# Kernel tuning notes

Measured on AMD Instinct MI355X. Metric: run time of the kernel, lower is better.

Reference implementation:

```python
import jax, jax.numpy as jnp
import numpy as np

N = 4096
IN_DIM, HID, OUT_DIM = 512, 256, 64
PROP_STEP = 10
LAM_HAT = 0.9
SCAD_A = 3.7
EPS = 1e-8


def setup_inputs() -> dict:
    key = jax.random.key(0)
    kA, kF, k1, k2 = jax.random.split(key, 4)
    # sparse symmetric 0/1 adjacency, zero diagonal (add_loops adds I later)
    u = jax.random.uniform(kA, (N, N), dtype=jnp.float32)
    A = (u < 0.005).astype(jnp.float32)
    A = jnp.maximum(A, A.T)
    A = A * (1.0 - jnp.eye(N, dtype=jnp.float32))
    F = jax.random.normal(kF, (N, IN_DIM), dtype=jnp.float32)
    W1 = jax.random.normal(k1, (IN_DIM, HID), dtype=jnp.float32) / np.sqrt(IN_DIM)
    b1 = jnp.zeros((HID,), dtype=jnp.float32)
    W2 = jax.random.normal(k2, (HID, OUT_DIM), dtype=jnp.float32) / np.sqrt(HID)
    b2 = jnp.zeros((OUT_DIM,), dtype=jnp.float32)
    raw_gamma = jnp.zeros((PROP_STEP,), dtype=jnp.float32)
    return {"A": A, "F": F, "W1": W1, "b1": b1, "W2": W2, "b2": b2,
            "raw_gamma": raw_gamma}


def reference(A, F, W1, b1, W2, b2, raw_gamma):
    lam = 1.0 / LAM_HAT - 1.0
    a = SCAD_A
    # MLP (dropout inactive at inference)
    F0 = jax.nn.relu(F @ W1 + b1) @ W2 + b2            # [N, out_dim]
    eye = jnp.eye(A.shape[0], dtype=A.dtype)
    A = A + eye                                        # add_loops
    D = A.sum(-1)                                      # [N]
    D_sq = jnp.sqrt(D)[:, None]                        # [N, 1]
    A_tilde = A / D_sq / D_sq.T                        # sym_norm: D^-1/2 A D^-1/2
    gammas = jax.nn.sigmoid(raw_gamma) * 2.0           # per-layer gamma in (0, 2)

    def step(Fc, gamma_k):
        Fn = Fc / D_sq
        nrm = jnp.linalg.norm(Fn, axis=-1, keepdims=True)
        Fu = Fn / jnp.maximum(nrm, 1e-12)
        # cosine distance in [0, 2]; detached as in torch (.detach())
        y = jax.lax.stop_gradient(1.0 - Fu @ Fu.T)     # [N, N]
        lam_k = jnp.maximum(gamma_k / a, EPS)
        t = a * lam_k
        safe_y = jnp.where(y <= 0.0, 1.0, y)
        w_mid = (t - y) / ((a - 1.0) * safe_y)
        # SCAD weight: 1 for y<=lam_k, linear decay on [lam_k, a*lam_k], 0 beyond
        W = jnp.where(y <= lam_k, 1.0, jnp.where(y <= t, w_mid, 0.0))
        W = W * (1.0 - eye)
        W = jnp.where(jnp.isnan(W), 1.0, W)
        Q_hat = ((W * A).sum(-1) / D + lam)[:, None]   # [N, 1]
        F_new = (W * A_tilde) @ Fc / Q_hat + lam * F0 / Q_hat
        return F_new, None

    F_out, _ = jax.lax.scan(step, F0, gammas)
    return F_out
```

## Files before the change

### kernel.cpp

```cpp
#include <hip/hip_runtime.h>
#include <hip/hip_bf16.h>

#define N_NODES 4096
#define IN_DIM  512
#define HID_DIM 256
#define OUT_DIM 64
#define PROP_STEP 10
#define MAX_DEG 128
#define KSPLIT  4
#define LAM_CONST (1.0f/0.9f - 1.0f)
#define SCAD_A 3.7f

__device__ __forceinline__ ushort f2bf(float f) {
    unsigned u = __float_as_uint(f);
    unsigned r = (u + 0x7FFFu + ((u >> 16) & 1u)) >> 16;
    return (ushort)r;
}
__device__ __forceinline__ unsigned pack2(float lo, float hi) {
    return (unsigned)f2bf(lo) | ((unsigned)f2bf(hi) << 16);
}
__device__ __forceinline__ float bflo(unsigned u) { return __uint_as_float(u << 16); }
__device__ __forceinline__ float bfhi(unsigned u) { return __uint_as_float(u & 0xFFFF0000u); }

__device__ __forceinline__ float wave_reduce_add(float v) {
#pragma unroll
    for (int off = 32; off > 0; off >>= 1) v += __shfl_xor(v, off, 64);
    return v;
}

__global__ __launch_bounds__(256) void build_graph(
    const float* __restrict__ A, int* __restrict__ ell, int* __restrict__ deg,
    float* __restrict__ invD, float* __restrict__ invDsq)
{
    int i = blockIdx.x;
    int t = threadIdx.x;
    __shared__ int cnt;
    if (t == 0) cnt = 0;
    __syncthreads();
    const float4* row = (const float4*)(A + (size_t)i * N_NODES);
    for (int q = t; q < N_NODES / 4; q += 256) {
        float4 v = row[q];
        if (v.x != 0.0f) { int p = atomicAdd(&cnt, 1); if (p < MAX_DEG) ell[i * MAX_DEG + p] = q * 4 + 0; }
        if (v.y != 0.0f) { int p = atomicAdd(&cnt, 1); if (p < MAX_DEG) ell[i * MAX_DEG + p] = q * 4 + 1; }
        if (v.z != 0.0f) { int p = atomicAdd(&cnt, 1); if (p < MAX_DEG) ell[i * MAX_DEG + p] = q * 4 + 2; }
        if (v.w != 0.0f) { int p = atomicAdd(&cnt, 1); if (p < MAX_DEG) ell[i * MAX_DEG + p] = q * 4 + 3; }
    }
    __syncthreads();
    if (t == 0) {
        int c = cnt;
        if (c > MAX_DEG) c = MAX_DEG;
        deg[i] = c;
        int pad = (c + 15) & ~15;
        if (pad > MAX_DEG) pad = MAX_DEG;
        for (int p = c; p < pad; p++) ell[i * MAX_DEG + p] = i;
        float d = (float)(cnt + 1);
        invD[i] = 1.0f / d;
        invDsq[i] = rsqrtf(d);
    }
}

__global__ __launch_bounds__(256) void mlp1(
    const float* __restrict__ F, const float* __restrict__ W1,
    float* __restrict__ Hp)
{
    __shared__ float sA[16][68];
    __shared__ float sB[16][68];
    int t  = threadIdx.x;
    int m0 = blockIdx.x * 64;
    int n0 = blockIdx.y * 64;
    int kp = blockIdx.z;
    int tm = (t & 15) * 4;
    int tn = (t >> 4) * 4;
    int ar = t >> 2;
    int ac = (t & 3) * 4;
    int br = t >> 4;
    int bc = (t & 15) * 4;
    float acc[4][4] = {};
    int k0 = kp * (IN_DIM / KSPLIT);
    for (int kc = k0; kc < k0 + IN_DIM / KSPLIT; kc += 16) {
        float4 va = *(const float4*)(F  + (size_t)(m0 + ar) * IN_DIM + kc + ac);
        float4 vb = *(const float4*)(W1 + (size_t)(kc + br) * HID_DIM + n0 + bc);
        __syncthreads();
        sA[ac + 0][ar] = va.x;
        sA[ac + 1][ar] = va.y;
        sA[ac + 2][ar] = va.z;
        sA[ac + 3][ar] = va.w;
        *(float4*)&sB[br][bc] = vb;
        __syncthreads();
#pragma unroll
        for (int k = 0; k < 16; k++) {
            float4 a = *(const float4*)&sA[k][tm];
            float4 b = *(const float4*)&sB[k][tn];
            acc[0][0] += a.x * b.x; acc[0][1] += a.x * b.y; acc[0][2] += a.x * b.z; acc[0][3] += a.x * b.w;
            acc[1][0] += a.y * b.x; acc[1][1] += a.y * b.y; acc[1][2] += a.y * b.z; acc[1][3] += a.y * b.w;
            acc[2][0] += a.z * b.x; acc[2][1] += a.z * b.y; acc[2][2] += a.z * b.z; acc[2][3] += a.z * b.w;
            acc[3][0] += a.w * b.x; acc[3][1] += a.w * b.y; acc[3][2] += a.w * b.z; acc[3][3] += a.w * b.w;
        }
    }
    float* Hb = Hp + (size_t)kp * N_NODES * HID_DIM;
#pragma unroll
    for (int r = 0; r < 4; r++) {
        *(float4*)&Hb[(size_t)(m0 + tm + r) * HID_DIM + n0 + tn] =
            make_float4(acc[r][0], acc[r][1], acc[r][2], acc[r][3]);
    }
}

__global__ __launch_bounds__(256) void reduce_H(
    float* __restrict__ Hp, const float* __restrict__ b1)
{
    size_t idx = (size_t)blockIdx.x * 256 + threadIdx.x;
    const size_t PS = (size_t)N_NODES * HID_DIM / 4;
    float4* H4 = (float4*)Hp;
    float4 s0 = H4[idx], s1 = H4[idx + PS], s2 = H4[idx + 2 * PS], s3 = H4[idx + 3 * PS];
    int col4 = (int)((idx * 4) & (HID_DIM - 1));
    float4 bb = *(const float4*)(b1 + col4);
    float4 o;
    o.x = fmaxf(s0.x + s1.x + s2.x + s3.x + bb.x, 0.0f);
    o.y = fmaxf(s0.y + s1.y + s2.y + s3.y + bb.y, 0.0f);
    o.z = fmaxf(s0.z + s1.z + s2.z + s3.z + bb.z, 0.0f);
    o.w = fmaxf(s0.w + s1.w + s2.w + s3.w + bb.w, 0.0f);
    H4[idx] = o;
}

__global__ __launch_bounds__(256) void mlp2(
    const float* __restrict__ H, const float* __restrict__ W2,
    const float* __restrict__ b2, const float* __restrict__ invDsq,
    float* __restrict__ F0, unsigned* __restrict__ P0)
{
    int wid = threadIdx.x >> 6, lane = threadIdx.x & 63;
    int row = blockIdx.x * 4 + wid;
    const float* h = H + (size_t)row * HID_DIM;
    float acc = b2[lane];
    for (int k = 0; k < HID_DIM; k += 4) {
        float4 hv = *(const float4*)(h + k);
        acc += hv.x * W2[(k + 0) * OUT_DIM + lane];
        acc += hv.y * W2[(k + 1) * OUT_DIM + lane];
        acc += hv.z * W2[(k + 2) * OUT_DIM + lane];
        acc += hv.w * W2[(k + 3) * OUT_DIM + lane];
    }
    size_t o = (size_t)row * OUT_DIM + lane;
    F0[o] = acc;
    float fn = acc * invDsq[row];
    float nrm = sqrtf(wave_reduce_add(fn * fn));
    float fu = fn / fmaxf(nrm, 1e-12f);
    float fu_hi = __shfl_xor(fu, 1, 64);
    float fn_hi = __shfl_xor(fn, 1, 64);
    if ((lane & 1) == 0) {
        unsigned* pr = P0 + (size_t)row * 64;
        pr[lane >> 1]        = pack2(fu, fu_hi);
        pr[32 + (lane >> 1)] = pack2(fn, fn_hi);
    }
}

__global__ __launch_bounds__(256) void propagate(
    const unsigned* __restrict__ Pin, const float* __restrict__ F0,
    const int* __restrict__ ell, const int* __restrict__ deg,
    const float* __restrict__ invD, const float* __restrict__ invDsq,
    const float* __restrict__ raw_gamma, int step,
    unsigned* __restrict__ Pout, float* __restrict__ FcOut,
    int writeNext, int writeOut)
{
    int lane = threadIdx.x & 63;
    int wid  = threadIdx.x >> 6;
    int r    = __builtin_amdgcn_readfirstlane(blockIdx.x * 4 + wid);
    int g    = lane >> 3;
    int sl   = lane & 7;

    float gamma = 2.0f / (1.0f + expf(-raw_gamma[step]));
    float lam_k = fmaxf(gamma / SCAD_A, 1e-8f);
    float tt    = SCAD_A * lam_k;
    const float inv_am1 = 1.0f / (SCAD_A - 1.0f);

    uint4 up = *(const uint4*)(Pin + (size_t)r * 64 + sl * 4);
    float ui[8] = { bflo(up.x), bfhi(up.x), bflo(up.y), bfhi(up.y),
                    bflo(up.z), bfhi(up.z), bflo(up.w), bfhi(up.w) };

    int dg = deg[r];
    int npair = (dg + 15) >> 4;
    const int* nb = ell + (size_t)r * MAX_DEG;

    float acc[8] = {};
    float qsum = 0.0f;

    for (int it = 0; it < npair; ++it) {
        int e0 = it * 16 + g;
        int e1 = e0 + 8;
        int j0 = nb[e0];
        int j1 = nb[e1];
        const unsigned* p0 = Pin + (size_t)j0 * 64 + sl * 4;
        const unsigned* p1 = Pin + (size_t)j1 * 64 + sl * 4;
        uint4 u0 = *(const uint4*)(p0);
        uint4 n0 = *(const uint4*)(p0 + 32);
        uint4 u1 = *(const uint4*)(p1);
        uint4 n1 = *(const uint4*)(p1 + 32);

        float pa = ui[0] * bflo(u0.x) + ui[1] * bfhi(u0.x) + ui[2] * bflo(u0.y) + ui[3] * bfhi(u0.y)
                 + ui[4] * bflo(u0.z) + ui[5] * bfhi(u0.z) + ui[6] * bflo(u0.w) + ui[7] * bfhi(u0.w);
        float pb = ui[0] * bflo(u1.x) + ui[1] * bfhi(u1.x) + ui[2] * bflo(u1.y) + ui[3] * bfhi(u1.y)
                 + ui[4] * bflo(u1.z) + ui[5] * bfhi(u1.z) + ui[6] * bflo(u1.w) + ui[7] * bfhi(u1.w);
        pa += __shfl_xor(pa, 1, 64); pb += __shfl_xor(pb, 1, 64);
        pa += __shfl_xor(pa, 2, 64); pb += __shfl_xor(pb, 2, 64);
        pa += __shfl_xor(pa, 4, 64); pb += __shfl_xor(pb, 4, 64);
        float ya = 1.0f - pa, yb = 1.0f - pb;
        float wa = (ya <= lam_k) ? 1.0f : ((ya <= tt) ? (tt - ya) * inv_am1 / ya : 0.0f);
        float wb = (yb <= lam_k) ? 1.0f : ((yb <= tt) ? (tt - yb) * inv_am1 / yb : 0.0f);
        if (e0 >= dg) wa = 0.0f;
        if (e1 >= dg) wb = 0.0f;
        acc[0] += wa * bflo(n0.x) + wb * bflo(n1.x);
        acc[1] += wa * bfhi(n0.x) + wb * bfhi(n1.x);
        acc[2] += wa * bflo(n0.y) + wb * bflo(n1.y);
        acc[3] += wa * bfhi(n0.y) + wb * bfhi(n1.y);
        acc[4] += wa * bflo(n0.z) + wb * bflo(n1.z);
        acc[5] += wa * bfhi(n0.z) + wb * bfhi(n1.z);
        acc[6] += wa * bflo(n0.w) + wb * bflo(n1.w);
        acc[7] += wa * bfhi(n0.w) + wb * bfhi(n1.w);
        qsum += wa + wb;
    }

#pragma unroll
    for (int off = 8; off <= 32; off <<= 1) {
#pragma unroll
        for (int q = 0; q < 8; q++) acc[q] += __shfl_xor(acc[q], off, 64);
        qsum += __shfl_xor(qsum, off, 64);
    }

    float iDs = invDsq[r];
    float Qh  = qsum * invD[r] + LAM_CONST;
    float rQh = 1.0f / Qh;
    const float4* f04 = (const float4*)(F0 + (size_t)r * OUT_DIM + sl * 8);
    float4 f0a = f04[0], f0b = f04[1];
    float f0v[8] = { f0a.x, f0a.y, f0a.z, f0a.w, f0b.x, f0b.y, f0b.z, f0b.w };
    float res[8];
#pragma unroll
    for (int q = 0; q < 8; q++) res[q] = (acc[q] * iDs + LAM_CONST * f0v[q]) * rQh;

    if (writeOut && lane < 8) {
        float4* o4 = (float4*)(FcOut + (size_t)r * OUT_DIM + sl * 8);
        o4[0] = make_float4(res[0], res[1], res[2], res[3]);
        o4[1] = make_float4(res[4], res[5], res[6], res[7]);
    }
    if (writeNext) {
        float fn[8];
        float ssq = 0.0f;
#pragma unroll
        for (int q = 0; q < 8; q++) { fn[q] = res[q] * iDs; ssq += fn[q] * fn[q]; }
        ssq += __shfl_xor(ssq, 1, 64);
        ssq += __shfl_xor(ssq, 2, 64);
        ssq += __shfl_xor(ssq, 4, 64);
        float inv_n = 1.0f / fmaxf(sqrtf(ssq), 1e-12f);
        if (lane < 8) {
            unsigned* pr = Pout + (size_t)r * 64 + sl * 4;
            uint4 fuPk, fnPk;
            fuPk.x = pack2(fn[0] * inv_n, fn[1] * inv_n);
            fuPk.y = pack2(fn[2] * inv_n, fn[3] * inv_n);
            fuPk.z = pack2(fn[4] * inv_n, fn[5] * inv_n);
            fuPk.w = pack2(fn[6] * inv_n, fn[7] * inv_n);
            fnPk.x = pack2(fn[0], fn[1]);
            fnPk.y = pack2(fn[2], fn[3]);
            fnPk.z = pack2(fn[4], fn[5]);
            fnPk.w = pack2(fn[6], fn[7]);
            *(uint4*)(pr)      = fuPk;
            *(uint4*)(pr + 32) = fnPk;
        }
    }
}

extern "C" void kernel_launch(void* const* d_in, const int* in_sizes, int n_in,
                              void* d_out, int out_size, void* d_ws, size_t ws_size,
                              hipStream_t stream)
{
    const float* A  = (const float*)d_in[0];
    const float* F  = (const float*)d_in[1];
    const float* W1 = (const float*)d_in[2];
    const float* b1 = (const float*)d_in[3];
    const float* W2 = (const float*)d_in[4];
    const float* b2 = (const float*)d_in[5];
    const float* rg = (const float*)d_in[6];
    float* out = (float*)d_out;

    char* p = (char*)d_ws;
    float* Hp     = (float*)p; p += (size_t)KSPLIT * N_NODES * HID_DIM * 4;
    float* F0     = (float*)p; p += (size_t)N_NODES * OUT_DIM * 4;
    unsigned* PB[2];
    PB[0] = (unsigned*)p; p += (size_t)N_NODES * 64 * 4;
    PB[1] = (unsigned*)p; p += (size_t)N_NODES * 64 * 4;
    float* invD   = (float*)p; p += (size_t)N_NODES * 4;
    float* invDsq = (float*)p; p += (size_t)N_NODES * 4;
    int*   deg    = (int*)p;   p += (size_t)N_NODES * 4;
    int*   ell    = (int*)p;   p += (size_t)N_NODES * MAX_DEG * 4;

    build_graph<<<N_NODES, 256, 0, stream>>>(A, ell, deg, invD, invDsq);
    mlp1<<<dim3(N_NODES / 64, HID_DIM / 64, KSPLIT), 256, 0, stream>>>(F, W1, Hp);
    reduce_H<<<N_NODES * HID_DIM / 4 / 256, 256, 0, stream>>>(Hp, b1);
    mlp2<<<N_NODES / 4, 256, 0, stream>>>(Hp, W2, b2, invDsq, F0, PB[0]);

    for (int k = 0; k < PROP_STEP; k++) {
        int in = k & 1, nx = (k + 1) & 1;
        int last = (k == PROP_STEP - 1);
        propagate<<<N_NODES / 4, 256, 0, stream>>>(
            PB[in], F0, ell, deg, invD, invDsq, rg, k,
            PB[nx], out, !last, last);
    }
}
```

Measured before the change: 232.1 us.

## Store only unit vectors plus norms, split neighbours across two waves per row

The per-node payload is cut from two bf16 vectors (unit and scaled features) to the unit vector plus one float norm, so the gather reads roughly half the bytes per neighbour. Fn is rebuilt as norm times the unit vector. Each row is now handled by two waves that take alternating neighbour chunks and combine their partial sums through shared memory. Neighbour indices are preloaded into lanes and shared with shuffles. This adds a block barrier and slightly more bf16 rounding error in Fn, and half the waves sit idle in the epilogue.

```diff
diff --git a/kernel.cpp b/kernel.cpp
--- a/kernel.cpp
+++ b/kernel.cpp
@@ -125,7 +125,7 @@
 __global__ __launch_bounds__(256) void mlp2(
     const float* __restrict__ H, const float* __restrict__ W2,
     const float* __restrict__ b2, const float* __restrict__ invDsq,
-    float* __restrict__ F0, unsigned* __restrict__ P0)
+    float* __restrict__ F0, unsigned* __restrict__ P0, float* __restrict__ nrm0)
 {
     int wid = threadIdx.x >> 6, lane = threadIdx.x & 63;
     int row = blockIdx.x * 4 + wid;
@@ -141,58 +141,61 @@
     size_t o = (size_t)row * OUT_DIM + lane;
     F0[o] = acc;
     float fn = acc * invDsq[row];
-    float nrm = sqrtf(wave_reduce_add(fn * fn));
-    float fu = fn / fmaxf(nrm, 1e-12f);
+    float nrm = fmaxf(sqrtf(wave_reduce_add(fn * fn)), 1e-12f);
+    float fu = fn / nrm;
     float fu_hi = __shfl_xor(fu, 1, 64);
-    float fn_hi = __shfl_xor(fn, 1, 64);
     if ((lane & 1) == 0) {
-        unsigned* pr = P0 + (size_t)row * 64;
-        pr[lane >> 1]        = pack2(fu, fu_hi);
-        pr[32 + (lane >> 1)] = pack2(fn, fn_hi);
-    }
-}
-
-__global__ __launch_bounds__(256) void propagate(
-    const unsigned* __restrict__ Pin, const float* __restrict__ F0,
+        P0[(size_t)row * 32 + (lane >> 1)] = pack2(fu, fu_hi);
+    }
+    if (lane == 0) nrm0[row] = nrm;
+}
+
+__global__ __launch_bounds__(256, 8) void propagate(
+    const unsigned* __restrict__ Pin, const float* __restrict__ nrmIn,
+    const float* __restrict__ F0,
     const int* __restrict__ ell, const int* __restrict__ deg,
     const float* __restrict__ invD, const float* __restrict__ invDsq,
     const float* __restrict__ raw_gamma, int step,
-    unsigned* __restrict__ Pout, float* __restrict__ FcOut,
-    int writeNext, int writeOut)
-{
+    unsigned* __restrict__ Pout, float* __restrict__ nrmOut,
+    float* __restrict__ FcOut, int writeNext, int writeOut)
+{
+    __shared__ float part[2][8][10];
     int lane = threadIdx.x & 63;
     int wid  = threadIdx.x >> 6;
-    int r    = __builtin_amdgcn_readfirstlane(blockIdx.x * 4 + wid);
+    int h    = wid & 1;
+    int rl   = wid >> 1;
+    int r    = __builtin_amdgcn_readfirstlane(blockIdx.x * 2 + rl);
     int g    = lane >> 3;
     int sl   = lane & 7;
+    const float inv_am1 = 1.0f / (SCAD_A - 1.0f);
 
     float gamma = 2.0f / (1.0f + expf(-raw_gamma[step]));
     float lam_k = fmaxf(gamma / SCAD_A, 1e-8f);
     float tt    = SCAD_A * lam_k;
-    const float inv_am1 = 1.0f / (SCAD_A - 1.0f);
-
-    uint4 up = *(const uint4*)(Pin + (size_t)r * 64 + sl * 4);
+
+    int dg = deg[r];
+    int pad = (dg + 15) & ~15;
+    int npair = pad >> 4;
+    const int* nb = ell + (size_t)r * MAX_DEG;
+    int ed0 = (lane < pad)      ? nb[lane]      : r;
+    int ed1 = (64 + lane < pad) ? nb[64 + lane] : r;
+
+    uint4 up = *(const uint4*)(Pin + (size_t)r * 32 + sl * 4);
     float ui[8] = { bflo(up.x), bfhi(up.x), bflo(up.y), bfhi(up.y),
                     bflo(up.z), bfhi(up.z), bflo(up.w), bfhi(up.w) };
 
-    int dg = deg[r];
-    int npair = (dg + 15) >> 4;
-    const int* nb = ell + (size_t)r * MAX_DEG;
-
     float acc[8] = {};
     float qsum = 0.0f;
-
-    for (int it = 0; it < npair; ++it) {
+    for (int it = h; it < npair; it += 2) {
         int e0 = it * 16 + g;
         int e1 = e0 + 8;
-        int j0 = nb[e0];
-        int j1 = nb[e1];
-        const unsigned* p0 = Pin + (size_t)j0 * 64 + sl * 4;
-        const unsigned* p1 = Pin + (size_t)j1 * 64 + sl * 4;
-        uint4 u0 = *(const uint4*)(p0);
-        uint4 n0 = *(const uint4*)(p0 + 32);
-        uint4 u1 = *(const uint4*)(p1);
-        uint4 n1 = *(const uint4*)(p1 + 32);
+        int src = (it < 4) ? ed0 : ed1;
+        int j0 = __shfl(src, e0 & 63, 64);
+        int j1 = __shfl(src, e1 & 63, 64);
+        uint4 u0 = *(const uint4*)(Pin + (size_t)j0 * 32 + sl * 4);
+        uint4 u1 = *(const uint4*)(Pin + (size_t)j1 * 32 + sl * 4);
+        float nr0 = nrmIn[j0];
+        float nr1 = nrmIn[j1];
 
         float pa = ui[0] * bflo(u0.x) + ui[1] * bfhi(u0.x) + ui[2] * bflo(u0.y) + ui[3] * bfhi(u0.y)
                  + ui[4] * bflo(u0.z) + ui[5] * bfhi(u0.z) + ui[6] * bflo(u0.w) + ui[7] * bfhi(u0.w);
@@ -206,15 +209,17 @@
         float wb = (yb <= lam_k) ? 1.0f : ((yb <= tt) ? (tt - yb) * inv_am1 / yb : 0.0f);
         if (e0 >= dg) wa = 0.0f;
         if (e1 >= dg) wb = 0.0f;
-        acc[0] += wa * bflo(n0.x) + wb * bflo(n1.x);
-        acc[1] += wa * bfhi(n0.x) + wb * bfhi(n1.x);
-        acc[2] += wa * bflo(n0.y) + wb * bflo(n1.y);
-        acc[3] += wa * bfhi(n0.y) + wb * bfhi(n1.y);
-        acc[4] += wa * bflo(n0.z) + wb * bflo(n1.z);
-        acc[5] += wa * bfhi(n0.z) + wb * bfhi(n1.z);
-        acc[6] += wa * bflo(n0.w) + wb * bflo(n1.w);
-        acc[7] += wa * bfhi(n0.w) + wb * bfhi(n1.w);
         qsum += wa + wb;
+        float wsa = wa * nr0;
+        float wsb = wb * nr1;
+        acc[0] += wsa * bflo(u0.x) + wsb * bflo(u1.x);
+        acc[1] += wsa * bfhi(u0.x) + wsb * bfhi(u1.x);
+        acc[2] += wsa * bflo(u0.y) + wsb * bflo(u1.y);
+        acc[3] += wsa * bfhi(u0.y) + wsb * bfhi(u1.y);
+        acc[4] += wsa * bflo(u0.z) + wsb * bflo(u1.z);
+        acc[5] += wsa * bfhi(u0.z) + wsb * bfhi(u1.z);
+        acc[6] += wsa * bflo(u0.w) + wsb * bflo(u1.w);
+        acc[7] += wsa * bfhi(u0.w) + wsb * bfhi(u1.w);
     }
 
 #pragma unroll
@@ -222,6 +227,19 @@
 #pragma unroll
         for (int q = 0; q < 8; q++) acc[q] += __shfl_xor(acc[q], off, 64);
         qsum += __shfl_xor(qsum, off, 64);
+    }
+
+    if (h == 1 && lane < 8) {
+#pragma unroll
+        for (int q = 0; q < 8; q++) part[rl][sl][q] = acc[q];
+        part[rl][sl][8] = qsum;
+    }
+    __syncthreads();
+    if (h == 1) return;
+    if (lane < 8) {
+#pragma unroll
+        for (int q = 0; q < 8; q++) acc[q] += part[rl][sl][q];
+        qsum += part[rl][sl][8];
     }
 
     float iDs = invDsq[r];
@@ -247,21 +265,17 @@
         ssq += __shfl_xor(ssq, 1, 64);
         ssq += __shfl_xor(ssq, 2, 64);
         ssq += __shfl_xor(ssq, 4, 64);
-        float inv_n = 1.0f / fmaxf(sqrtf(ssq), 1e-12f);
+        float nrm = fmaxf(sqrtf(ssq), 1e-12f);
+        float inv_n = 1.0f / nrm;
         if (lane < 8) {
-            unsigned* pr = Pout + (size_t)r * 64 + sl * 4;
-            uint4 fuPk, fnPk;
+            uint4 fuPk;
             fuPk.x = pack2(fn[0] * inv_n, fn[1] * inv_n);
             fuPk.y = pack2(fn[2] * inv_n, fn[3] * inv_n);
             fuPk.z = pack2(fn[4] * inv_n, fn[5] * inv_n);
             fuPk.w = pack2(fn[6] * inv_n, fn[7] * inv_n);
-            fnPk.x = pack2(fn[0], fn[1]);
-            fnPk.y = pack2(fn[2], fn[3]);
-            fnPk.z = pack2(fn[4], fn[5]);
-            fnPk.w = pack2(fn[6], fn[7]);
-            *(uint4*)(pr)      = fuPk;
-            *(uint4*)(pr + 32) = fnPk;
+            *(uint4*)(Pout + (size_t)r * 32 + sl * 4) = fuPk;
         }
+        if (lane == 0) nrmOut[r] = nrm;
     }
 }
 
@@ -281,9 +295,10 @@
     char* p = (char*)d_ws;
     float* Hp     = (float*)p; p += (size_t)KSPLIT * N_NODES * HID_DIM * 4;
     float* F0     = (float*)p; p += (size_t)N_NODES * OUT_DIM * 4;
-    unsigned* PB[2];
-    PB[0] = (unsigned*)p; p += (size_t)N_NODES * 64 * 4;
-    PB[1] = (unsigned*)p; p += (size_t)N_NODES * 64 * 4;
+    unsigned* Pa  = (unsigned*)p; p += (size_t)N_NODES * 32 * 4;
+    unsigned* Pb  = (unsigned*)p; p += (size_t)N_NODES * 32 * 4;
+    float* nrmA   = (float*)p; p += (size_t)N_NODES * 4;
+    float* nrmB   = (float*)p; p += (size_t)N_NODES * 4;
     float* invD   = (float*)p; p += (size_t)N_NODES * 4;
     float* invDsq = (float*)p; p += (size_t)N_NODES * 4;
     int*   deg    = (int*)p;   p += (size_t)N_NODES * 4;
@@ -292,13 +307,16 @@
     build_graph<<<N_NODES, 256, 0, stream>>>(A, ell, deg, invD, invDsq);
     mlp1<<<dim3(N_NODES / 64, HID_DIM / 64, KSPLIT), 256, 0, stream>>>(F, W1, Hp);
     reduce_H<<<N_NODES * HID_DIM / 4 / 256, 256, 0, stream>>>(Hp, b1);
-    mlp2<<<N_NODES / 4, 256, 0, stream>>>(Hp, W2, b2, invDsq, F0, PB[0]);
+    mlp2<<<N_NODES / 4, 256, 0, stream>>>(Hp, W2, b2, invDsq, F0, Pa, nrmA);
 
     for (int k = 0; k < PROP_STEP; k++) {
-        int in = k & 1, nx = (k + 1) & 1;
+        unsigned* Pin   = (k & 1) ? Pb : Pa;
+        unsigned* Pout  = (k & 1) ? Pa : Pb;
+        float* nIn      = (k & 1) ? nrmB : nrmA;
+        float* nOut     = (k & 1) ? nrmA : nrmB;
         int last = (k == PROP_STEP - 1);
-        propagate<<<N_NODES / 4, 256, 0, stream>>>(
-            PB[in], F0, ell, deg, invD, invDsq, rg, k,
-            PB[nx], out, !last, last);
-    }
-}
+        propagate<<<N_NODES / 2, 256, 0, stream>>>(
+            Pin, nIn, F0, ell, deg, invD, invDsq, rg, k,
+            Pout, nOut, out, !last, last);
+    }
+}
```

New measurement: 231.4 us. About the same (-0.3%).
